# Kernel tuning notes

Hardware: AMD Instinct MI355X
Metric: run time of the kernel (lower is better)

## Reference

```python
import jax, jax.numpy as jnp
import numpy as np

B, H, N, D = 8, 12, 1024, 64
SCALE = 1.0 / float(np.sqrt(D))  # 0.125; torch forward default is 1.0 but 1/sqrt(d) is the production value
EPS = 1e-06


def setup_inputs() -> dict:
    key = jax.random.key(0)
    kq, kk, kv = jax.random.split(key, 3)
    q = jax.random.normal(kq, (B, H, N, D), dtype=jnp.float32)
    k = jax.random.normal(kk, (B, H, N, D), dtype=jnp.float32)
    v = jax.random.normal(kv, (B, H, N, D), dtype=jnp.float32)
    # Parameter init per L2Q.__init__: alpha=0.125, beta=0.5, gamma=1/n_tokens
    alpha = jnp.full((H, 1, 1), 0.125, dtype=jnp.float32)
    beta = jnp.full((H, 1, 1), 0.5, dtype=jnp.float32)
    gamma = jnp.full((H, 1, 1), 1.0 / N, dtype=jnp.float32)
    return {"q": q, "k": k, "v": v, "alpha": alpha, "beta": beta, "gamma": gamma}


def reference(q, k, v, alpha, beta, gamma):
    # logits: (B, H, N, N)
    logits = jnp.einsum("bhnd,bhmd->bhnm", q, k) * SCALE
    # per-head quadratic polynomial, then ReLU; params (H,1,1) broadcast over (B,H,N,N)
    attn = jax.nn.relu(alpha * logits * logits + beta * logits + gamma)
    attn = attn / (jnp.sum(attn, axis=-1, keepdims=True) + EPS)
    return jnp.einsum("bhnm,bhmd->bhnd", attn, v)
```

## Files before the change

kernel.cpp:

```cpp
#include <hip/hip_runtime.h>
#include <hip/hip_bf16.h>

typedef __attribute__((ext_vector_type(8))) short bf16x8;
typedef __attribute__((ext_vector_type(4))) float f32x4;

#define MFMA16(a, b, c) __builtin_amdgcn_mfma_f32_16x16x32_bf16(a, b, c, 0, 0, 0)

static constexpr int kH = 12;
static constexpr int kN = 1024;
static constexpr int kD = 64;
static constexpr int kBH = 96;
static constexpr int kND = kN * kD;
static constexpr int kTiles = kN / 64;
static constexpr float kScale = 0.125f;
static constexpr float kEps = 1e-6f;
static constexpr long kTensorElems = (long)kBH * kND;
static constexpr long kWsNeeded = 3 * kTensorElems * 2;

__device__ __forceinline__ unsigned bfbits(float x) {
    union { __hip_bfloat16 h; unsigned short u; } c;
    c.h = __float2bfloat16(x);
    return (unsigned)c.u;
}
__device__ __forceinline__ unsigned pack2_rne(float a, float b) {
    return bfbits(a) | (bfbits(b) << 16);
}
__device__ __forceinline__ unsigned pack2_rhu(float lo, float hi) {
    unsigned a = __builtin_bit_cast(unsigned, lo) + 0x8000u;
    unsigned b = __builtin_bit_cast(unsigned, hi) + 0x8000u;
    return __builtin_amdgcn_perm(b, a, 0x07060302u);
}

__device__ __forceinline__ void gl_lds16(const void* g, void* l) {
    __builtin_amdgcn_global_load_lds(
        (const __attribute__((address_space(1))) void*)g,
        (__attribute__((address_space(3))) void*)l, 16, 0, 0);
}

__global__ __launch_bounds__(256, 4) void cast_qk(
    const float* __restrict__ q, const float* __restrict__ k,
    unsigned* __restrict__ qo, unsigned* __restrict__ ko)
{
    const int tid = blockIdx.x * 256 + threadIdx.x;
    const int stride = 1536 * 256;
    const long perT = kTensorElems / 4;
#pragma unroll
    for (int r = 0; r < 8; ++r) {
        long i = (long)tid + (long)r * stride;
        const float4* src; unsigned* dst; long j;
        if (i < perT) { src = (const float4*)q; dst = qo; j = i; }
        else          { src = (const float4*)k; dst = ko; j = i - perT; }
        float4 f = src[j];
        uint2 u;
        u.x = pack2_rne(f.x, f.y);
        u.y = pack2_rne(f.z, f.w);
        *(uint2*)&dst[j * 2] = u;
    }
}

__global__ __launch_bounds__(256, 4) void vtrans(
    const float* __restrict__ v, unsigned* __restrict__ vt)
{
    static constexpr int TS = 68;
    __shared__ float T32[64 * TS];
    const int bid = blockIdx.x;
    const int bh = bid >> 4, kt = bid & 15;
    const int t = threadIdx.x;
    const float* vp = v + (long)bh * kND + (long)kt * 64 * kD;

#pragma unroll
    for (int r = 0; r < 4; ++r) {
        const int f4 = t + 256 * r;
        const int n = f4 >> 4, d4 = f4 & 15;
        const float4 f = *(const float4*)(vp + (long)n * kD + 4 * d4);
        *(float4*)&T32[n * TS + 4 * d4] = f;
    }
    __syncthreads();

    const int d = t >> 2, c = t & 3;
    unsigned u[8];
#pragma unroll
    for (int j = 0; j < 8; ++j) {
        const int key = c * 16 + 2 * j;
        u[j] = pack2_rne(T32[key * TS + d], T32[(key + 1) * TS + d]);
    }
    unsigned* dst = vt + (long)bh * (kND / 2) + (long)d * (kN / 2) + kt * 32 + c * 8;
    *(uint4*)(dst)     = *(uint4*)&u[0];
    *(uint4*)(dst + 4) = *(uint4*)&u[4];
}

__global__ __launch_bounds__(256, 3) void l2q_main(
    const unsigned short* __restrict__ qbf, const unsigned short* __restrict__ kbf,
    const unsigned short* __restrict__ vtbf,
    const float* __restrict__ alpha, const float* __restrict__ beta, const float* __restrict__ gamma,
    float* __restrict__ out)
{
    __shared__ __align__(16) unsigned Ks[2][2048];
    __shared__ __align__(16) unsigned Vs[2][2048];
    __shared__ __align__(16) unsigned Pu[4][1024];

    const int bid  = blockIdx.x;
    const int bh   = bid >> 3;
    const int qt   = bid & 7;
    const int h    = bh % kH;
    const int t    = threadIdx.x;
    const int wave = t >> 6;
    const int lane = t & 63;
    const int quad = lane >> 4;
    const int l15  = lane & 15;
    const int sw   = l15 & 7;

    const float al = alpha[h] * (kScale * kScale);
    const float be = beta[h] * kScale;
    const float ga = gamma[h];

    const unsigned short* qp = qbf + (long)bh * kND;
    const unsigned short* kp = kbf + (long)bh * kND;
    const unsigned short* vp = vtbf + (long)bh * kND;

    bf16x8 qa[2][2];
#pragma unroll
    for (int qb = 0; qb < 2; ++qb) {
        const int row = qt * 128 + wave * 32 + qb * 16 + l15;
#pragma unroll
        for (int kc = 0; kc < 2; ++kc)
            qa[qb][kc] = *(const bf16x8*)(qp + (long)row * kD + kc * 32 + quad * 8);
    }

    f32x4 oacc[2][4];
#pragma unroll
    for (int qb = 0; qb < 2; ++qb)
#pragma unroll
        for (int db = 0; db < 4; ++db)
            oacc[qb][db] = (f32x4){0.f, 0.f, 0.f, 0.f};
    f32x4 dsv[2] = {(f32x4){0.f,0.f,0.f,0.f}, (f32x4){0.f,0.f,0.f,0.f}};

    const int srow = lane >> 3;
    const int g    = lane & 7;
    auto stageKV = [&](int buf, int tile) {
        const int k0 = tile * 64;
#pragma unroll
        for (int c = 0; c < 2; ++c) {
            const int r  = (c * 4 + wave) * 8 + srow;
            const int gl = (g ^ (r & 7)) * 8;
            gl_lds16(kp + (long)(k0 + r) * kD + gl, &Ks[buf][(c * 4 + wave) * 256]);
            gl_lds16(vp + (long)r * kN + k0 + gl,   &Vs[buf][(c * 4 + wave) * 256]);
        }
    };

    stageKV(0, 0);

    unsigned* Pw = Pu[wave];

    for (int tile = 0; tile < kTiles; ++tile) {
        const int buf = tile & 1;
        __syncthreads();
        if (tile + 1 < kTiles) stageKV(buf ^ 1, tile + 1);

        const unsigned* Kb = Ks[buf];
        const unsigned* Vb = Vs[buf];

        f32x4 st[2][4];
#pragma unroll
        for (int qb = 0; qb < 2; ++qb)
#pragma unroll
            for (int kb = 0; kb < 4; ++kb)
                st[qb][kb] = (f32x4){0.f, 0.f, 0.f, 0.f};
#pragma unroll
        for (int kb = 0; kb < 4; ++kb) {
            const int row = kb * 16 + l15;
            bf16x8 kf0 = *(const bf16x8*)&Kb[row * 32 + ((quad ^ sw) << 2)];
            bf16x8 kf1 = *(const bf16x8*)&Kb[row * 32 + (((4 + quad) ^ sw) << 2)];
#pragma unroll
            for (int qb = 0; qb < 2; ++qb) {
                st[qb][kb] = MFMA16(kf0, qa[qb][0], st[qb][kb]);
                st[qb][kb] = MFMA16(kf1, qa[qb][1], st[qb][kb]);
            }
        }

#pragma unroll
        for (int qb = 0; qb < 2; ++qb) {
            const int pbase = (qb * 16 + l15) * 32;
#pragma unroll
            for (int kb = 0; kb < 4; ++kb) {
                f32x4 s = st[qb][kb];
                f32x4 w = s * al + be;
                w = w * s + ga;
                w[0] = fmaxf(w[0], 0.f); w[1] = fmaxf(w[1], 0.f);
                w[2] = fmaxf(w[2], 0.f); w[3] = fmaxf(w[3], 0.f);
                dsv[qb] += w;
                uint2 pk2;
                pk2.x = pack2_rhu(w[0], w[1]);
                pk2.y = pack2_rhu(w[2], w[3]);
                const int col = kb * 8 + quad * 2;
                const int gr = col >> 2, off = col & 3;
                *(uint2*)&Pw[pbase + ((gr ^ sw) << 2) + off] = pk2;
            }
        }

        bf16x8 pf[2][2];
#pragma unroll
        for (int qb = 0; qb < 2; ++qb) {
            const int pbase = (qb * 16 + l15) * 32;
            pf[qb][0] = *(const bf16x8*)&Pw[pbase + ((quad ^ sw) << 2)];
            pf[qb][1] = *(const bf16x8*)&Pw[pbase + (((4 + quad) ^ sw) << 2)];
        }
#pragma unroll
        for (int db = 0; db < 4; ++db) {
            const int vrow = db * 16 + l15;
            bf16x8 vf0 = *(const bf16x8*)&Vb[vrow * 32 + ((quad ^ sw) << 2)];
            bf16x8 vf1 = *(const bf16x8*)&Vb[vrow * 32 + (((4 + quad) ^ sw) << 2)];
#pragma unroll
            for (int qb = 0; qb < 2; ++qb) {
                oacc[qb][db] = MFMA16(pf[qb][0], vf0, oacc[qb][db]);
                oacc[qb][db] = MFMA16(pf[qb][1], vf1, oacc[qb][db]);
            }
        }
    }

    float dr[2];
#pragma unroll
    for (int qb = 0; qb < 2; ++qb) {
        float d = dsv[qb][0] + dsv[qb][1] + dsv[qb][2] + dsv[qb][3];
        d += __shfl_xor(d, 16);
        d += __shfl_xor(d, 32);
        dr[qb] = 1.0f / (d + kEps);
    }

    const long obase = (long)bh * kND;
#pragma unroll
    for (int qb = 0; qb < 2; ++qb)
#pragma unroll
        for (int i = 0; i < 4; ++i) {
            const float rr = __shfl(dr[qb], quad * 4 + i);
            const int row = qt * 128 + wave * 32 + qb * 16 + quad * 4 + i;
#pragma unroll
            for (int db = 0; db < 4; ++db)
                out[obase + (long)row * kD + db * 16 + l15] = oacc[qb][db][i] * rr;
        }
}

static constexpr int KSU = 36;
static constexpr int VSU = 36;
static constexpr int PSU = 36;

__global__ __launch_bounds__(256, 3) void l2q_attn_fb(
    const float* __restrict__ q, const float* __restrict__ k, const float* __restrict__ v,
    const float* __restrict__ alpha, const float* __restrict__ beta, const float* __restrict__ gamma,
    float* __restrict__ out)
{
    __shared__ __align__(16) unsigned KsU[64 * KSU];
    __shared__ __align__(16) unsigned VtU[64 * VSU];
    __shared__ __align__(16) unsigned PU[128 * PSU];

    const int bid  = blockIdx.x;
    const int bh   = bid >> 3;
    const int qt   = bid & 7;
    const int h    = bh % kH;
    const int t    = threadIdx.x;
    const int wave = t >> 6;
    const int lane = t & 63;
    const int quad = lane >> 4;
    const int l15  = lane & 15;

    const float al = alpha[h], be = beta[h], ga = gamma[h];

    const long base = (long)bh * kN * kD;
    const float* qp = q + base;
    const float* kp = k + base;
    const float* vp = v + base;

    bf16x8 qa[2][2];
#pragma unroll
    for (int rb = 0; rb < 2; ++rb) {
        const int row = qt * 128 + wave * 32 + rb * 16 + l15;
#pragma unroll
        for (int kc = 0; kc < 2; ++kc) {
            const float* src = qp + (long)row * kD + kc * 32 + quad * 8;
            const float4 f0 = *(const float4*)(src);
            const float4 f1 = *(const float4*)(src + 4);
            bf16x8 a;
            a[0] = (short)bfbits(f0.x); a[1] = (short)bfbits(f0.y);
            a[2] = (short)bfbits(f0.z); a[3] = (short)bfbits(f0.w);
            a[4] = (short)bfbits(f1.x); a[5] = (short)bfbits(f1.y);
            a[6] = (short)bfbits(f1.z); a[7] = (short)bfbits(f1.w);
            qa[rb][kc] = a;
        }
    }

    f32x4 oacc[2][4];
#pragma unroll
    for (int rb = 0; rb < 2; ++rb)
#pragma unroll
        for (int db = 0; db < 4; ++db)
            oacc[rb][db] = (f32x4){0.f, 0.f, 0.f, 0.f};

    float dsum[2][4] = {{0.f, 0.f, 0.f, 0.f}, {0.f, 0.f, 0.f, 0.f}};
    unsigned* Pw = &PU[wave * 32 * PSU];

    for (int tile = 0; tile < kTiles; ++tile) {
        __syncthreads();
        const int k0 = tile * 64;
#pragma unroll
        for (int r = 0; r < 4; ++r) {
            const int f4 = t + 256 * r;
            const int n = f4 >> 4, d4 = f4 & 15;
            const float4 kg = *(const float4*)(kp + (long)(k0 + n) * kD + 4 * d4);
            uint2 pk;
            pk.x = pack2_rne(kg.x, kg.y);
            pk.y = pack2_rne(kg.z, kg.w);
            *(uint2*)&KsU[n * KSU + 2 * d4] = pk;
        }
#pragma unroll
        for (int r = 0; r < 2; ++r) {
            const int u = t + 256 * r;
            const int key2 = u & 31, d4 = u >> 5;
            const float* s0 = vp + (long)(k0 + 2 * key2) * kD + 4 * d4;
            const float4 va = *(const float4*)(s0);
            const float4 vb = *(const float4*)(s0 + kD);
            VtU[(4 * d4 + 0) * VSU + key2] = pack2_rne(va.x, vb.x);
            VtU[(4 * d4 + 1) * VSU + key2] = pack2_rne(va.y, vb.y);
            VtU[(4 * d4 + 2) * VSU + key2] = pack2_rne(va.z, vb.z);
            VtU[(4 * d4 + 3) * VSU + key2] = pack2_rne(va.w, vb.w);
        }
        __syncthreads();

        f32x4 s[2][4];
#pragma unroll
        for (int rb = 0; rb < 2; ++rb)
#pragma unroll
            for (int nb = 0; nb < 4; ++nb)
                s[rb][nb] = (f32x4){0.f, 0.f, 0.f, 0.f};
#pragma unroll
        for (int nb = 0; nb < 4; ++nb) {
            bf16x8 kb0 = *(const bf16x8*)&KsU[(nb * 16 + l15) * KSU + 4 * quad];
            bf16x8 kb1 = *(const bf16x8*)&KsU[(nb * 16 + l15) * KSU + 16 + 4 * quad];
#pragma unroll
            for (int rb = 0; rb < 2; ++rb) {
                s[rb][nb] = MFMA16(qa[rb][0], kb0, s[rb][nb]);
                s[rb][nb] = MFMA16(qa[rb][1], kb1, s[rb][nb]);
            }
        }

        const bool ev = (lane & 1) == 0;
#pragma unroll
        for (int rb = 0; rb < 2; ++rb) {
#pragma unroll
            for (int nb = 0; nb < 4; ++nb) {
                float w0, w1, w2, w3;
                {
                    float l0 = s[rb][nb][0] * kScale;
                    float l1 = s[rb][nb][1] * kScale;
                    float l2 = s[rb][nb][2] * kScale;
                    float l3 = s[rb][nb][3] * kScale;
                    w0 = fmaxf(fmaf(fmaf(al, l0, be), l0, ga), 0.f);
                    w1 = fmaxf(fmaf(fmaf(al, l1, be), l1, ga), 0.f);
                    w2 = fmaxf(fmaf(fmaf(al, l2, be), l2, ga), 0.f);
                    w3 = fmaxf(fmaf(fmaf(al, l3, be), l3, ga), 0.f);
                }
                dsum[rb][0] += w0; dsum[rb][1] += w1;
                dsum[rb][2] += w2; dsum[rb][3] += w3;

                const float o0 = __shfl_xor(w0, 1);
                const float o1 = __shfl_xor(w1, 1);
                const float o2 = __shfl_xor(w2, 1);
                const float o3 = __shfl_xor(w3, 1);
                const unsigned pa = ev ? pack2_rne(w0, o0) : pack2_rne(o2, w2);
                const unsigned pb = ev ? pack2_rne(w1, o1) : pack2_rne(o3, w3);
                const int r0 = ev ? 0 : 2;
                const int cu = (16 * nb + (l15 & ~1)) >> 1;
                const int rowb = rb * 16 + quad * 4 + r0;
                Pw[rowb * PSU + cu] = pa;
                Pw[(rowb + 1) * PSU + cu] = pb;
            }
        }

        bf16x8 pf[2][2];
#pragma unroll
        for (int rb = 0; rb < 2; ++rb)
#pragma unroll
            for (int kc = 0; kc < 2; ++kc)
                pf[rb][kc] = *(const bf16x8*)&Pw[(rb * 16 + l15) * PSU + 16 * kc + 4 * quad];
#pragma unroll
        for (int db = 0; db < 4; ++db) {
            bf16x8 vf0 = *(const bf16x8*)&VtU[(db * 16 + l15) * VSU + 4 * quad];
            bf16x8 vf1 = *(const bf16x8*)&VtU[(db * 16 + l15) * VSU + 16 + 4 * quad];
#pragma unroll
            for (int rb = 0; rb < 2; ++rb) {
                oacc[rb][db] = MFMA16(pf[rb][0], vf0, oacc[rb][db]);
                oacc[rb][db] = MFMA16(pf[rb][1], vf1, oacc[rb][db]);
            }
        }
    }

#pragma unroll
    for (int rb = 0; rb < 2; ++rb)
#pragma unroll
        for (int i = 0; i < 4; ++i) {
            float d = dsum[rb][i];
            d += __shfl_xor(d, 1);
            d += __shfl_xor(d, 2);
            d += __shfl_xor(d, 4);
            d += __shfl_xor(d, 8);
            dsum[rb][i] = 1.0f / (d + kEps);
        }

#pragma unroll
    for (int rb = 0; rb < 2; ++rb)
#pragma unroll
        for (int db = 0; db < 4; ++db)
#pragma unroll
            for (int i = 0; i < 4; ++i) {
                const int row = qt * 128 + wave * 32 + rb * 16 + quad * 4 + i;
                out[base + (long)row * kD + db * 16 + l15] = oacc[rb][db][i] * dsum[rb][i];
            }
}

extern "C" void kernel_launch(void* const* d_in, const int* in_sizes, int n_in,
                              void* d_out, int out_size, void* d_ws, size_t ws_size,
                              hipStream_t stream) {
    const float* q     = (const float*)d_in[0];
    const float* k     = (const float*)d_in[1];
    const float* v     = (const float*)d_in[2];
    const float* alpha = (const float*)d_in[3];
    const float* beta  = (const float*)d_in[4];
    const float* gamma = (const float*)d_in[5];
    float* out = (float*)d_out;

    if (ws_size < (size_t)kWsNeeded) {
        l2q_attn_fb<<<dim3(768), dim3(256), 0, stream>>>(q, k, v, alpha, beta, gamma, out);
        return;
    }

    unsigned* qbf = (unsigned*)d_ws;
    unsigned* kbf = qbf + kTensorElems / 2;
    unsigned* vtb = kbf + kTensorElems / 2;

    cast_qk<<<dim3(1536), dim3(256), 0, stream>>>(q, k, qbf, kbf);
    vtrans<<<dim3(1536), dim3(256), 0, stream>>>(v, vtb);
    l2q_main<<<dim3(768), dim3(256), 0, stream>>>(
        (const unsigned short*)qbf, (const unsigned short*)kbf, (const unsigned short*)vtb,
        alpha, beta, gamma, out);
}
```

Measured before the change: 158.5 us.

## Fuse K cast into V transpose, cast Q in-kernel, shrink key tiles to 32

The separate Q/K cast kernel is removed. K conversion is merged into the V-transpose prep kernel, and Q is converted to bf16 directly inside the main attention kernel, which drops one launch and one workspace round trip. The main kernel now streams 32-key tiles with half-size LDS buffers, launch bounds raised to 5 blocks per CU, and an XCD-aware block-to-head mapping for L2 locality. The trade is twice as many loop iterations and barriers per block in exchange for higher occupancy and less global traffic.

Measured after the change: 157.9 us. About the same (-0.3%).

```diff
diff --git a/kernel.cpp b/kernel.cpp
--- a/kernel.cpp
+++ b/kernel.cpp
@@ -11,11 +11,11 @@
 static constexpr int kD = 64;
 static constexpr int kBH = 96;
 static constexpr int kND = kN * kD;
-static constexpr int kTiles = kN / 64;
+static constexpr int kTiles = kN / 32;
 static constexpr float kScale = 0.125f;
 static constexpr float kEps = 1e-6f;
 static constexpr long kTensorElems = (long)kBH * kND;
-static constexpr long kWsNeeded = 3 * kTensorElems * 2;
+static constexpr long kWsNeeded = 2 * kTensorElems * 2;
 
 __device__ __forceinline__ unsigned bfbits(float x) {
     union { __hip_bfloat16 h; unsigned short u; } c;
@@ -30,44 +30,35 @@
     unsigned b = __builtin_bit_cast(unsigned, hi) + 0x8000u;
     return __builtin_amdgcn_perm(b, a, 0x07060302u);
 }
-
 __device__ __forceinline__ void gl_lds16(const void* g, void* l) {
     __builtin_amdgcn_global_load_lds(
         (const __attribute__((address_space(1))) void*)g,
         (__attribute__((address_space(3))) void*)l, 16, 0, 0);
 }
 
-__global__ __launch_bounds__(256, 4) void cast_qk(
-    const float* __restrict__ q, const float* __restrict__ k,
-    unsigned* __restrict__ qo, unsigned* __restrict__ ko)
-{
-    const int tid = blockIdx.x * 256 + threadIdx.x;
-    const int stride = 1536 * 256;
-    const long perT = kTensorElems / 4;
-#pragma unroll
-    for (int r = 0; r < 8; ++r) {
-        long i = (long)tid + (long)r * stride;
-        const float4* src; unsigned* dst; long j;
-        if (i < perT) { src = (const float4*)q; dst = qo; j = i; }
-        else          { src = (const float4*)k; dst = ko; j = i - perT; }
-        float4 f = src[j];
-        uint2 u;
-        u.x = pack2_rne(f.x, f.y);
-        u.y = pack2_rne(f.z, f.w);
-        *(uint2*)&dst[j * 2] = u;
-    }
-}
-
-__global__ __launch_bounds__(256, 4) void vtrans(
-    const float* __restrict__ v, unsigned* __restrict__ vt)
+__global__ __launch_bounds__(256, 2) void prep(
+    const float* __restrict__ k, const float* __restrict__ v,
+    unsigned* __restrict__ kbf, unsigned* __restrict__ vtb)
 {
     static constexpr int TS = 68;
     __shared__ float T32[64 * TS];
     const int bid = blockIdx.x;
-    const int bh = bid >> 4, kt = bid & 15;
+    const int bh = bid >> 4, nt = bid & 15;
     const int t = threadIdx.x;
-    const float* vp = v + (long)bh * kND + (long)kt * 64 * kD;
-
+
+    const float* kp = k + (long)bh * kND + (long)nt * 64 * kD;
+    unsigned* ko = kbf + ((long)bh * kND + (long)nt * 64 * kD) / 2;
+#pragma unroll
+    for (int r = 0; r < 4; ++r) {
+        const int f4 = t + 256 * r;
+        const float4 f = ((const float4*)kp)[f4];
+        uint2 u;
+        u.x = pack2_rne(f.x, f.y);
+        u.y = pack2_rne(f.z, f.w);
+        *(uint2*)&ko[f4 * 2] = u;
+    }
+
+    const float* vp = v + (long)bh * kND + (long)nt * 64 * kD;
 #pragma unroll
     for (int r = 0; r < 4; ++r) {
         const int f4 = t + 256 * r;
@@ -76,7 +67,6 @@
         *(float4*)&T32[n * TS + 4 * d4] = f;
     }
     __syncthreads();
-
     const int d = t >> 2, c = t & 3;
     unsigned u[8];
 #pragma unroll
@@ -84,20 +74,173 @@
         const int key = c * 16 + 2 * j;
         u[j] = pack2_rne(T32[key * TS + d], T32[(key + 1) * TS + d]);
     }
-    unsigned* dst = vt + (long)bh * (kND / 2) + (long)d * (kN / 2) + kt * 32 + c * 8;
+    unsigned* dst = vtb + (long)bh * (kND / 2) + (long)d * (kN / 2) + nt * 32 + c * 8;
     *(uint4*)(dst)     = *(uint4*)&u[0];
     *(uint4*)(dst + 4) = *(uint4*)&u[4];
 }
 
-__global__ __launch_bounds__(256, 3) void l2q_main(
-    const unsigned short* __restrict__ qbf, const unsigned short* __restrict__ kbf,
-    const unsigned short* __restrict__ vtbf,
+__global__ __launch_bounds__(256, 5) void l2q_main(
+    const float* __restrict__ q,
+    const unsigned short* __restrict__ kbf, const unsigned short* __restrict__ vtbf,
     const float* __restrict__ alpha, const float* __restrict__ beta, const float* __restrict__ gamma,
     float* __restrict__ out)
 {
-    __shared__ __align__(16) unsigned Ks[2][2048];
-    __shared__ __align__(16) unsigned Vs[2][2048];
-    __shared__ __align__(16) unsigned Pu[4][1024];
+    __shared__ __align__(16) unsigned Ks[2][1024];
+    __shared__ __align__(16) unsigned Vs[2][1024];
+    __shared__ __align__(16) unsigned Pu[4][512];
+
+    const int bid  = blockIdx.x;
+    const int xcd  = bid & 7;
+    const int s    = bid >> 3;
+    const int bh   = xcd * 12 + (s % 12);
+    const int qt   = s / 12;
+    const int h    = bh % kH;
+    const int t    = threadIdx.x;
+    const int wave = t >> 6;
+    const int lane = t & 63;
+    const int quad = lane >> 4;
+    const int l15  = lane & 15;
+
+    const float al = alpha[h] * (kScale * kScale);
+    const float be = beta[h] * kScale;
+    const float ga = gamma[h];
+
+    const float* qp = q + (long)bh * kND;
+    const unsigned short* kp = kbf + (long)bh * kND;
+    const unsigned short* vp = vtbf + (long)bh * kND;
+
+    bf16x8 qa[2][2];
+#pragma unroll
+    for (int qb = 0; qb < 2; ++qb) {
+        const int row = qt * 128 + wave * 32 + qb * 16 + l15;
+#pragma unroll
+        for (int kc = 0; kc < 2; ++kc) {
+            const float* src = qp + (long)row * kD + kc * 32 + quad * 8;
+            const float4 f0 = *(const float4*)(src);
+            const float4 f1 = *(const float4*)(src + 4);
+            uint4 u;
+            u.x = pack2_rne(f0.x, f0.y);
+            u.y = pack2_rne(f0.z, f0.w);
+            u.z = pack2_rne(f1.x, f1.y);
+            u.w = pack2_rne(f1.z, f1.w);
+            qa[qb][kc] = __builtin_bit_cast(bf16x8, u);
+        }
+    }
+
+    f32x4 oacc[2][4];
+#pragma unroll
+    for (int qb = 0; qb < 2; ++qb)
+#pragma unroll
+        for (int db = 0; db < 4; ++db)
+            oacc[qb][db] = (f32x4){0.f, 0.f, 0.f, 0.f};
+    f32x4 dsv[2] = {(f32x4){0.f,0.f,0.f,0.f}, (f32x4){0.f,0.f,0.f,0.f}};
+
+    const int krow = wave * 8 + (lane >> 3);
+    const int kgl  = (((lane & 7) ^ (krow & 7))) * 8;
+    const int vrow = wave * 16 + (lane >> 2);
+    const int vgl  = (((lane & 3) ^ (vrow & 3))) * 8;
+    auto stageKV = [&](int buf, int tile) {
+        const int k0 = tile * 32;
+        gl_lds16(kp + (long)(k0 + krow) * kD + kgl, &Ks[buf][wave * 256]);
+        gl_lds16(vp + (long)vrow * kN + k0 + vgl,   &Vs[buf][wave * 256]);
+    };
+
+    stageKV(0, 0);
+    unsigned* Pw = Pu[wave];
+    const int sw3 = l15 & 3, sw7 = l15 & 7;
+
+    for (int tile = 0; tile < kTiles; ++tile) {
+        const int buf = tile & 1;
+        __syncthreads();
+        if (tile + 1 < kTiles) stageKV(buf ^ 1, tile + 1);
+
+        const unsigned* Kb = Ks[buf];
+        const unsigned* Vb = Vs[buf];
+
+        f32x4 st[2][2];
+#pragma unroll
+        for (int qb = 0; qb < 2; ++qb)
+#pragma unroll
+            for (int kb = 0; kb < 2; ++kb)
+                st[qb][kb] = (f32x4){0.f, 0.f, 0.f, 0.f};
+#pragma unroll
+        for (int kb = 0; kb < 2; ++kb) {
+            const int row = (kb * 16 + l15) * 32;
+            bf16x8 kf0 = *(const bf16x8*)&Kb[row + ((quad ^ sw7) << 2)];
+            bf16x8 kf1 = *(const bf16x8*)&Kb[row + (((4 + quad) ^ sw7) << 2)];
+#pragma unroll
+            for (int qb = 0; qb < 2; ++qb) {
+                st[qb][kb] = MFMA16(kf0, qa[qb][0], st[qb][kb]);
+                st[qb][kb] = MFMA16(kf1, qa[qb][1], st[qb][kb]);
+            }
+        }
+
+#pragma unroll
+        for (int qb = 0; qb < 2; ++qb) {
+            const int pbase = (qb * 16 + l15) * 16;
+#pragma unroll
+            for (int kb = 0; kb < 2; ++kb) {
+                f32x4 sfr = st[qb][kb];
+                f32x4 w = sfr * al + be;
+                w = w * sfr + ga;
+                w[0] = fmaxf(w[0], 0.f); w[1] = fmaxf(w[1], 0.f);
+                w[2] = fmaxf(w[2], 0.f); w[3] = fmaxf(w[3], 0.f);
+                dsv[qb] += w;
+                uint2 pk2;
+                pk2.x = pack2_rhu(w[0], w[1]);
+                pk2.y = pack2_rhu(w[2], w[3]);
+                const int gr = kb * 2 + (quad >> 1);
+                *(uint2*)&Pw[pbase + ((gr ^ sw3) << 2) + (quad & 1) * 2] = pk2;
+            }
+        }
+        __asm__ __volatile__("" ::: "memory");
+
+        bf16x8 pf[2];
+        pf[0] = *(const bf16x8*)&Pw[(l15)      * 16 + ((quad ^ sw3) << 2)];
+        pf[1] = *(const bf16x8*)&Pw[(16 + l15) * 16 + ((quad ^ sw3) << 2)];
+#pragma unroll
+        for (int db = 0; db < 4; ++db) {
+            bf16x8 vf = *(const bf16x8*)&Vb[(db * 16 + l15) * 16 + ((quad ^ sw3) << 2)];
+            oacc[0][db] = MFMA16(pf[0], vf, oacc[0][db]);
+            oacc[1][db] = MFMA16(pf[1], vf, oacc[1][db]);
+        }
+        __asm__ __volatile__("" ::: "memory");
+    }
+
+    float dr[2];
+#pragma unroll
+    for (int qb = 0; qb < 2; ++qb) {
+        float d = dsv[qb][0] + dsv[qb][1] + dsv[qb][2] + dsv[qb][3];
+        d += __shfl_xor(d, 16);
+        d += __shfl_xor(d, 32);
+        dr[qb] = 1.0f / (d + kEps);
+    }
+
+    const long obase = (long)bh * kND;
+#pragma unroll
+    for (int qb = 0; qb < 2; ++qb)
+#pragma unroll
+        for (int i = 0; i < 4; ++i) {
+            const float rr = __shfl(dr[qb], quad * 4 + i);
+            const int row = qt * 128 + wave * 32 + qb * 16 + quad * 4 + i;
+#pragma unroll
+            for (int db = 0; db < 4; ++db)
+                out[obase + (long)row * kD + db * 16 + l15] = oacc[qb][db][i] * rr;
+        }
+}
+
+static constexpr int KSU = 36;
+static constexpr int VSU = 36;
+static constexpr int PSU = 36;
+
+__global__ __launch_bounds__(256, 3) void l2q_attn_fb(
+    const float* __restrict__ q, const float* __restrict__ k, const float* __restrict__ v,
+    const float* __restrict__ alpha, const float* __restrict__ beta, const float* __restrict__ gamma,
+    float* __restrict__ out)
+{
+    __shared__ __align__(16) unsigned KsU[64 * KSU];
+    __shared__ __align__(16) unsigned VtU[64 * VSU];
+    __shared__ __align__(16) unsigned PU[128 * PSU];
 
     const int bid  = blockIdx.x;
     const int bh   = bid >> 3;
@@ -108,160 +251,6 @@
     const int lane = t & 63;
     const int quad = lane >> 4;
     const int l15  = lane & 15;
-    const int sw   = l15 & 7;
-
-    const float al = alpha[h] * (kScale * kScale);
-    const float be = beta[h] * kScale;
-    const float ga = gamma[h];
-
-    const unsigned short* qp = qbf + (long)bh * kND;
-    const unsigned short* kp = kbf + (long)bh * kND;
-    const unsigned short* vp = vtbf + (long)bh * kND;
-
-    bf16x8 qa[2][2];
-#pragma unroll
-    for (int qb = 0; qb < 2; ++qb) {
-        const int row = qt * 128 + wave * 32 + qb * 16 + l15;
-#pragma unroll
-        for (int kc = 0; kc < 2; ++kc)
-            qa[qb][kc] = *(const bf16x8*)(qp + (long)row * kD + kc * 32 + quad * 8);
-    }
-
-    f32x4 oacc[2][4];
-#pragma unroll
-    for (int qb = 0; qb < 2; ++qb)
-#pragma unroll
-        for (int db = 0; db < 4; ++db)
-            oacc[qb][db] = (f32x4){0.f, 0.f, 0.f, 0.f};
-    f32x4 dsv[2] = {(f32x4){0.f,0.f,0.f,0.f}, (f32x4){0.f,0.f,0.f,0.f}};
-
-    const int srow = lane >> 3;
-    const int g    = lane & 7;
-    auto stageKV = [&](int buf, int tile) {
-        const int k0 = tile * 64;
-#pragma unroll
-        for (int c = 0; c < 2; ++c) {
-            const int r  = (c * 4 + wave) * 8 + srow;
-            const int gl = (g ^ (r & 7)) * 8;
-            gl_lds16(kp + (long)(k0 + r) * kD + gl, &Ks[buf][(c * 4 + wave) * 256]);
-            gl_lds16(vp + (long)r * kN + k0 + gl,   &Vs[buf][(c * 4 + wave) * 256]);
-        }
-    };
-
-    stageKV(0, 0);
-
-    unsigned* Pw = Pu[wave];
-
-    for (int tile = 0; tile < kTiles; ++tile) {
-        const int buf = tile & 1;
-        __syncthreads();
-        if (tile + 1 < kTiles) stageKV(buf ^ 1, tile + 1);
-
-        const unsigned* Kb = Ks[buf];
-        const unsigned* Vb = Vs[buf];
-
-        f32x4 st[2][4];
-#pragma unroll
-        for (int qb = 0; qb < 2; ++qb)
-#pragma unroll
-            for (int kb = 0; kb < 4; ++kb)
-                st[qb][kb] = (f32x4){0.f, 0.f, 0.f, 0.f};
-#pragma unroll
-        for (int kb = 0; kb < 4; ++kb) {
-            const int row = kb * 16 + l15;
-            bf16x8 kf0 = *(const bf16x8*)&Kb[row * 32 + ((quad ^ sw) << 2)];
-            bf16x8 kf1 = *(const bf16x8*)&Kb[row * 32 + (((4 + quad) ^ sw) << 2)];
-#pragma unroll
-            for (int qb = 0; qb < 2; ++qb) {
-                st[qb][kb] = MFMA16(kf0, qa[qb][0], st[qb][kb]);
-                st[qb][kb] = MFMA16(kf1, qa[qb][1], st[qb][kb]);
-            }
-        }
-
-#pragma unroll
-        for (int qb = 0; qb < 2; ++qb) {
-            const int pbase = (qb * 16 + l15) * 32;
-#pragma unroll
-            for (int kb = 0; kb < 4; ++kb) {
-                f32x4 s = st[qb][kb];
-                f32x4 w = s * al + be;
-                w = w * s + ga;
-                w[0] = fmaxf(w[0], 0.f); w[1] = fmaxf(w[1], 0.f);
-                w[2] = fmaxf(w[2], 0.f); w[3] = fmaxf(w[3], 0.f);
-                dsv[qb] += w;
-                uint2 pk2;
-                pk2.x = pack2_rhu(w[0], w[1]);
-                pk2.y = pack2_rhu(w[2], w[3]);
-                const int col = kb * 8 + quad * 2;
-                const int gr = col >> 2, off = col & 3;
-                *(uint2*)&Pw[pbase + ((gr ^ sw) << 2) + off] = pk2;
-            }
-        }
-
-        bf16x8 pf[2][2];
-#pragma unroll
-        for (int qb = 0; qb < 2; ++qb) {
-            const int pbase = (qb * 16 + l15) * 32;
-            pf[qb][0] = *(const bf16x8*)&Pw[pbase + ((quad ^ sw) << 2)];
-            pf[qb][1] = *(const bf16x8*)&Pw[pbase + (((4 + quad) ^ sw) << 2)];
-        }
-#pragma unroll
-        for (int db = 0; db < 4; ++db) {
-            const int vrow = db * 16 + l15;
-            bf16x8 vf0 = *(const bf16x8*)&Vb[vrow * 32 + ((quad ^ sw) << 2)];
-            bf16x8 vf1 = *(const bf16x8*)&Vb[vrow * 32 + (((4 + quad) ^ sw) << 2)];
-#pragma unroll
-            for (int qb = 0; qb < 2; ++qb) {
-                oacc[qb][db] = MFMA16(pf[qb][0], vf0, oacc[qb][db]);
-                oacc[qb][db] = MFMA16(pf[qb][1], vf1, oacc[qb][db]);
-            }
-        }
-    }
-
-    float dr[2];
-#pragma unroll
-    for (int qb = 0; qb < 2; ++qb) {
-        float d = dsv[qb][0] + dsv[qb][1] + dsv[qb][2] + dsv[qb][3];
-        d += __shfl_xor(d, 16);
-        d += __shfl_xor(d, 32);
-        dr[qb] = 1.0f / (d + kEps);
-    }
-
-    const long obase = (long)bh * kND;
-#pragma unroll
-    for (int qb = 0; qb < 2; ++qb)
-#pragma unroll
-        for (int i = 0; i < 4; ++i) {
-            const float rr = __shfl(dr[qb], quad * 4 + i);
-            const int row = qt * 128 + wave * 32 + qb * 16 + quad * 4 + i;
-#pragma unroll
-            for (int db = 0; db < 4; ++db)
-                out[obase + (long)row * kD + db * 16 + l15] = oacc[qb][db][i] * rr;
-        }
-}
-
-static constexpr int KSU = 36;
-static constexpr int VSU = 36;
-static constexpr int PSU = 36;
-
-__global__ __launch_bounds__(256, 3) void l2q_attn_fb(
-    const float* __restrict__ q, const float* __restrict__ k, const float* __restrict__ v,
-    const float* __restrict__ alpha, const float* __restrict__ beta, const float* __restrict__ gamma,
-    float* __restrict__ out)
-{
-    __shared__ __align__(16) unsigned KsU[64 * KSU];
-    __shared__ __align__(16) unsigned VtU[64 * VSU];
-    __shared__ __align__(16) unsigned PU[128 * PSU];
-
-    const int bid  = blockIdx.x;
-    const int bh   = bid >> 3;
-    const int qt   = bid & 7;
-    const int h    = bh % kH;
-    const int t    = threadIdx.x;
-    const int wave = t >> 6;
-    const int lane = t & 63;
-    const int quad = lane >> 4;
-    const int l15  = lane & 15;
 
     const float al = alpha[h], be = beta[h], ga = gamma[h];
 
@@ -279,12 +268,12 @@
             const float* src = qp + (long)row * kD + kc * 32 + quad * 8;
             const float4 f0 = *(const float4*)(src);
             const float4 f1 = *(const float4*)(src + 4);
-            bf16x8 a;
-            a[0] = (short)bfbits(f0.x); a[1] = (short)bfbits(f0.y);
-            a[2] = (short)bfbits(f0.z); a[3] = (short)bfbits(f0.w);
-            a[4] = (short)bfbits(f1.x); a[5] = (short)bfbits(f1.y);
-            a[6] = (short)bfbits(f1.z); a[7] = (short)bfbits(f1.w);
-            qa[rb][kc] = a;
+            uint4 u;
+            u.x = pack2_rne(f0.x, f0.y);
+            u.y = pack2_rne(f0.z, f0.w);
+            u.z = pack2_rne(f1.x, f1.y);
+            u.w = pack2_rne(f1.z, f1.w);
+            qa[rb][kc] = __builtin_bit_cast(bf16x8, u);
         }
     }
 
@@ -298,7 +287,7 @@
     float dsum[2][4] = {{0.f, 0.f, 0.f, 0.f}, {0.f, 0.f, 0.f, 0.f}};
     unsigned* Pw = &PU[wave * 32 * PSU];
 
-    for (int tile = 0; tile < kTiles; ++tile) {
+    for (int tile = 0; tile < 16; ++tile) {
         __syncthreads();
         const int k0 = tile * 64;
 #pragma unroll
@@ -432,13 +421,11 @@
         return;
     }
 
-    unsigned* qbf = (unsigned*)d_ws;
-    unsigned* kbf = qbf + kTensorElems / 2;
+    unsigned* kbf = (unsigned*)d_ws;
     unsigned* vtb = kbf + kTensorElems / 2;
 
-    cast_qk<<<dim3(1536), dim3(256), 0, stream>>>(q, k, qbf, kbf);
-    vtrans<<<dim3(1536), dim3(256), 0, stream>>>(v, vtb);
+    prep<<<dim3(1536), dim3(256), 0, stream>>>(k, v, kbf, vtb);
     l2q_main<<<dim3(768), dim3(256), 0, stream>>>(
-        (const unsigned short*)qbf, (const unsigned short*)kbf, (const unsigned short*)vtb,
+        q, (const unsigned short*)kbf, (const unsigned short*)vtb,
         alpha, beta, gamma, out);
 }
```
